# Performance work log

Hardware: AMD Instinct MI355X
Metric: run time of the kernel (lower is better)

Reference implementation:

```python
import jax, jax.numpy as jnp
import numpy as np


def setup_inputs() -> dict:
    key = jax.random.key(0)
    ks = jax.random.split(key, 8)
    B, C, H, W = 4, 128, 128, 128
    C8 = C // 8
    x = jax.random.normal(ks[0], (B, C, H, W), jnp.float32)
    # 1x1 conv weights as [out, in] matrices + biases
    Wq = jax.random.normal(ks[1], (C8, C), jnp.float32) * 0.05
    bq = jax.random.normal(ks[2], (C8,), jnp.float32) * 0.01
    Wk = jax.random.normal(ks[3], (C8, C), jnp.float32) * 0.05
    bk = jax.random.normal(ks[4], (C8,), jnp.float32) * 0.01
    Wv = jax.random.normal(ks[5], (C, C), jnp.float32) * 0.05
    bv = jax.random.normal(ks[6], (C,), jnp.float32) * 0.01
    # nn.Parameter(torch.zeros(1)) in the original; use nonzero so output/grads are nontrivial
    gamma = jax.random.normal(ks[7], (), jnp.float32) * 0.1
    return {"x": x, "Wq": Wq, "bq": bq, "Wk": Wk, "bk": bk,
            "Wv": Wv, "bv": bv, "gamma": gamma}


def reference(x, Wq, bq, Wk, bk, Wv, bv, gamma):
    # x: [b, c, h, w]
    b, c, h, w = x.shape
    # 1x1 convs == channel contractions
    q = jnp.einsum('bchw,oc->bohw', x, Wq) + bq[None, :, None, None]  # [b,c8,h,w]
    k = jnp.einsum('bchw,oc->bohw', x, Wk) + bk[None, :, None, None]  # [b,c8,h,w]
    v = jnp.einsum('bchw,oc->bohw', x, Wv) + bv[None, :, None, None]  # [b,c, h,w]

    # column (height) attention logits: e_h[b, h1, w, h2], diagonal masked to -inf
    e_h = jnp.einsum('bcxw,bcyw->bxwy', q, k)
    diag = jnp.eye(h, dtype=bool)  # [h1, h2]
    e_h = jnp.where(diag[:, None, :], -jnp.inf, e_h)
    # row (width) attention logits: e_w[b, h, w1, w2]
    e_w = jnp.einsum('bchx,bchy->bhxy', q, k)

    # joint softmax over concatenated (h2 + w2) axis
    attn = jax.nn.softmax(jnp.concatenate([e_h, e_w], axis=3), axis=3)  # [b,h,w,h+w]
    attn_h = attn[..., :h]   # [b, h1, w, h2]
    attn_w = attn[..., h:]   # [b, h, w1, w2]

    # aggregate values along columns and rows
    out_h = jnp.einsum('bcyw,bxwy->bcxw', v, attn_h)  # [b,c,h,w]
    out_w = jnp.einsum('bchy,bhxy->bchx', v, attn_w)  # [b,c,h,w]

    out = gamma * (out_h + out_w) + x
    # return_attn: stack([b h2 h1 w, b w2 h w1], dim=1)
    return_attn = jnp.stack([jnp.transpose(attn_h, (0, 3, 1, 2)),
                             jnp.transpose(attn_w, (0, 3, 1, 2))], axis=1)
    return out, return_attn
```

## Files before the change

kernel.cpp:

```cpp
#include <hip/hip_runtime.h>
#include <math.h>

#define HW_ 16384
#define SLOT_ 2097152ULL
#define BSTR_ 4194304ULL

typedef __attribute__((ext_vector_type(8))) short short8v;
typedef __attribute__((ext_vector_type(4))) float f32x4;

__device__ __forceinline__ unsigned short f2bf(float f) {
  unsigned int u = __float_as_uint(f);
  u = (u + 0x7FFFu + ((u >> 16) & 1u)) >> 16;
  return (unsigned short)u;
}
__device__ __forceinline__ float bf2f(unsigned short h) {
  return __uint_as_float(((unsigned int)h) << 16);
}

__global__ void __launch_bounds__(256, 2)
qkv_proj(const float* __restrict__ x,
         const float* __restrict__ Wq, const float* __restrict__ bq,
         const float* __restrict__ Wk, const float* __restrict__ bk,
         const float* __restrict__ Wv, const float* __restrict__ bv,
         float* __restrict__ qT, float* __restrict__ kT,
         unsigned short* __restrict__ vA0,
         unsigned short* __restrict__ Ew, float* __restrict__ rsw) {
  __shared__ unsigned short LDSU[39168];
  unsigned short (*WqkL)[136] = (unsigned short(*)[136])LDSU;
  unsigned short (*WvL)[136]  = (unsigned short(*)[136])(LDSU + 4352);
  unsigned short (*XT)[136]   = (unsigned short(*)[136])(LDSU + 21760);
  int t = threadIdx.x;
  int blk = blockIdx.x;
  int b = blk >> 7, h = blk & 127;
  {
    int och = t >> 3, kb = (t & 7) * 16;
    const float* src = (och < 16 ? Wq + och * 128 : Wk + (och - 16) * 128) + kb;
    union { unsigned short us[8]; uint4 v; } p0, p1;
#pragma unroll
    for (int j = 0; j < 8; ++j) p0.us[j] = f2bf(src[j]);
#pragma unroll
    for (int j = 0; j < 8; ++j) p1.us[j] = f2bf(src[8 + j]);
    *(uint4*)&WqkL[och][kb]     = p0.v;
    *(uint4*)&WqkL[och][kb + 8] = p1.v;
  }
  {
    int c = t >> 1, kb = (t & 1) * 64;
    const float* src = Wv + c * 128 + kb;
#pragma unroll
    for (int g = 0; g < 8; ++g) {
      union { unsigned short us[8]; uint4 v; } p;
#pragma unroll
      for (int j = 0; j < 8; ++j) p.us[j] = f2bf(src[g * 8 + j]);
      *(uint4*)&WvL[c][kb + g * 8] = p.v;
    }
  }
  {
    int k = t >> 1, pxb = (t & 1) * 64;
    const float* src = x + (size_t)b * 128 * HW_ + (size_t)k * HW_ + h * 128 + pxb;
#pragma unroll
    for (int j = 0; j < 64; ++j)
      XT[pxb + j][k] = f2bf(src[j]);
  }
  int wv = t >> 6, l = t & 63;
  int lm = l & 15, lk = (l >> 4) * 4, lr4 = (l >> 4) * 4;
  int wc = (wv >> 1) * 64, wx = (wv & 1) * 64;
  int ocht = (wv >> 1) * 16;
  float bvr[4][4];
#pragma unroll
  for (int mi = 0; mi < 4; ++mi)
#pragma unroll
    for (int r = 0; r < 4; ++r) bvr[mi][r] = bv[wc + mi * 16 + lr4 + r];
  float bqk[4];
#pragma unroll
  for (int r = 0; r < 4; ++r) {
    int och = ocht + lr4 + r;
    bqk[r] = (och < 16) ? bq[och] : bk[och - 16];
  }
  f32x4 acc[4][4];
#pragma unroll
  for (int mi = 0; mi < 4; ++mi)
#pragma unroll
    for (int ni = 0; ni < 4; ++ni) acc[mi][ni] = (f32x4){0.f, 0.f, 0.f, 0.f};
  f32x4 acc2[4];
#pragma unroll
  for (int ni = 0; ni < 4; ++ni) acc2[ni] = (f32x4){0.f, 0.f, 0.f, 0.f};
  __syncthreads();
  for (int y0 = 0; y0 < 128; y0 += 32) {
    short8v bf[4];
#pragma unroll
    for (int ni = 0; ni < 4; ++ni) {
      const unsigned short* bp = &XT[wx + ni * 16 + lm][y0 + lk];
      union { uint2 p[2]; short8v v; } u;
      u.p[0] = *(const uint2*)bp;
      u.p[1] = *(const uint2*)(bp + 16);
      bf[ni] = u.v;
    }
#pragma unroll
    for (int mi = 0; mi < 4; ++mi) {
      const unsigned short* ap = &WvL[wc + mi * 16 + lm][y0 + lk];
      union { uint2 p[2]; short8v v; } u;
      u.p[0] = *(const uint2*)ap;
      u.p[1] = *(const uint2*)(ap + 16);
      short8v af = u.v;
#pragma unroll
      for (int ni = 0; ni < 4; ++ni)
        acc[mi][ni] = __builtin_amdgcn_mfma_f32_16x16x32_bf16(af, bf[ni], acc[mi][ni], 0, 0, 0);
    }
    {
      const unsigned short* ap = &WqkL[ocht + lm][y0 + lk];
      union { uint2 p[2]; short8v v; } u;
      u.p[0] = *(const uint2*)ap;
      u.p[1] = *(const uint2*)(ap + 16);
      short8v aq = u.v;
#pragma unroll
      for (int ni = 0; ni < 4; ++ni)
        acc2[ni] = __builtin_amdgcn_mfma_f32_16x16x32_bf16(aq, bf[ni], acc2[ni], 0, 0, 0);
    }
  }
#pragma unroll
  for (int ni = 0; ni < 4; ++ni) {
    int px = wx + ni * 16 + lm;
#pragma unroll
    for (int mi = 0; mi < 4; ++mi)
#pragma unroll
      for (int r = 0; r < 4; ++r) {
        int c = wc + mi * 16 + lr4 + r;
        vA0[(size_t)(b * 128 + h) * 16384 + (size_t)c * 128 + px] =
            f2bf(acc[mi][ni][r] + bvr[mi][r]);
      }
  }
  __syncthreads();
  float (*QKs)[36] = (float(*)[36])(LDSU + 21760);
#pragma unroll
  for (int ni = 0; ni < 4; ++ni) {
    int px = (wv & 1) * 64 + ni * 16 + lm;
#pragma unroll
    for (int r = 0; r < 4; ++r)
      QKs[px][ocht + lr4 + r] = acc2[ni][r] + bqk[r];
  }
  __syncthreads();
  {
    int px_ = t >> 1, sel = t & 1;
    const float* qr = &QKs[px_][sel * 16];
    float4 r0 = *(const float4*)(qr);
    float4 r1 = *(const float4*)(qr + 4);
    float4 r2 = *(const float4*)(qr + 8);
    float4 r3 = *(const float4*)(qr + 12);
    float* dstT = (sel ? kT : qT) + ((size_t)(b * HW_ + px_ * 128 + h)) * 16;
    *(float4*)(dstT)      = r0;
    *(float4*)(dstT + 4)  = r1;
    *(float4*)(dstT + 8)  = r2;
    *(float4*)(dstT + 12) = r3;
  }
  float (*Qs)[132] = (float(*)[132])(LDSU + 4352);
  float (*Ks)[132] = (float(*)[132])(LDSU + 8576);
  {
    int cc = t & 15, pb = (t >> 4) * 8;
#pragma unroll
    for (int u = 0; u < 8; ++u) {
      Qs[cc][pb + u] = QKs[pb + u][cc];
      Ks[cc][pb + u] = QKs[pb + u][16 + cc];
    }
  }
  __syncthreads();
  {
    int tr = (t >> 4) * 8;
    int ty = (t & 15) * 8;
    float sc_[8][8] = {{0.f}};
#pragma unroll
    for (int c = 0; c < 16; ++c) {
      float qa[8], ka[8];
      *(float4*)(qa)     = *(const float4*)&Qs[c][tr];
      *(float4*)(qa + 4) = *(const float4*)&Qs[c][tr + 4];
      *(float4*)(ka)     = *(const float4*)&Ks[c][ty];
      *(float4*)(ka + 4) = *(const float4*)&Ks[c][ty + 4];
#pragma unroll
      for (int u = 0; u < 8; ++u)
#pragma unroll
        for (int v = 0; v < 8; ++v)
          sc_[u][v] = fmaf(qa[u], ka[v], sc_[u][v]);
    }
    float rp[8];
#pragma unroll
    for (int u = 0; u < 8; ++u) {
      rp[u] = 0.f;
#pragma unroll
      for (int v = 0; v < 8; ++v) {
        float e = __expf(sc_[u][v]);
        sc_[u][v] = e;
        rp[u] += e;
      }
    }
    unsigned short* out = Ew + (size_t)blk * 16384;
#pragma unroll
    for (int u = 0; u < 8; ++u) {
      union { unsigned short us[8]; uint4 v; } pk;
#pragma unroll
      for (int v = 0; v < 8; ++v) pk.us[v] = f2bf(sc_[u][v]);
      *(uint4*)&out[(tr + u) * 128 + ty] = pk.v;
    }
#pragma unroll
    for (int u = 0; u < 8; ++u) {
      rp[u] += __shfl_xor(rp[u], 1);
      rp[u] += __shfl_xor(rp[u], 2);
      rp[u] += __shfl_xor(rp[u], 4);
      rp[u] += __shfl_xor(rp[u], 8);
    }
    if ((t & 15) == 0) {
#pragma unroll
      for (int u = 0; u < 8; ++u) rsw[(size_t)blk * 128 + tr + u] = rp[u];
    }
  }
}

__global__ void score_h(const float* __restrict__ Q, const float* __restrict__ K,
                        unsigned short* __restrict__ E, float* __restrict__ rsum,
                        size_t ebs, size_t eoff) {
  __shared__ float Qs[16][132];
  __shared__ float Ks[16][132];
  int slab = blockIdx.x;
  int b = slab >> 7, s = slab & 127;
  const float* qb = Q + (size_t)slab * 2048;
  const float* kb = K + (size_t)slab * 2048;
  int t = threadIdx.x;
  int cc = t & 15;
  int pb = (t >> 4) * 8;
#pragma unroll
  for (int u = 0; u < 8; ++u) {
    Qs[cc][pb + u] = qb[(size_t)(pb + u) * 16 + cc];
    Ks[cc][pb + u] = kb[(size_t)(pb + u) * 16 + cc];
  }
  __syncthreads();
  int tr = (t >> 4) * 8;
  int ty = (t & 15) * 8;
  float acc[8][8] = {{0.f}};
#pragma unroll
  for (int c = 0; c < 16; ++c) {
    float qa[8], ka[8];
    *(float4*)(qa)     = *(const float4*)&Qs[c][tr];
    *(float4*)(qa + 4) = *(const float4*)&Qs[c][tr + 4];
    *(float4*)(ka)     = *(const float4*)&Ks[c][ty];
    *(float4*)(ka + 4) = *(const float4*)&Ks[c][ty + 4];
#pragma unroll
    for (int u = 0; u < 8; ++u)
#pragma unroll
      for (int v = 0; v < 8; ++v)
        acc[u][v] = fmaf(qa[u], ka[v], acc[u][v]);
  }
  float rp[8];
#pragma unroll
  for (int u = 0; u < 8; ++u) {
    rp[u] = 0.f;
#pragma unroll
    for (int v = 0; v < 8; ++v) {
      float e = __expf(acc[u][v]);
      if ((tr + u) == (ty + v)) e = 0.f;
      acc[u][v] = e;
      rp[u] += e;
    }
  }
  unsigned short* out = E + (size_t)b * ebs + eoff + (size_t)s * 16384;
#pragma unroll
  for (int u = 0; u < 8; ++u) {
    union { unsigned short us[8]; uint4 v; } pk;
#pragma unroll
    for (int v = 0; v < 8; ++v) pk.us[v] = f2bf(acc[u][v]);
    *(uint4*)&out[(tr + u) * 128 + ty] = pk.v;
  }
#pragma unroll
  for (int u = 0; u < 8; ++u) {
    rp[u] += __shfl_xor(rp[u], 1);
    rp[u] += __shfl_xor(rp[u], 2);
    rp[u] += __shfl_xor(rp[u], 4);
    rp[u] += __shfl_xor(rp[u], 8);
  }
  if ((t & 15) == 0) {
#pragma unroll
    for (int u = 0; u < 8; ++u) rsum[(size_t)slab * 128 + tr + u] = rp[u];
  }
}

__global__ void trans_v(const unsigned short* __restrict__ vA0, unsigned short* __restrict__ vA1,
                        const float* __restrict__ rsw, const float* __restrict__ rsh,
                        float* __restrict__ dij, float* __restrict__ dji) {
  __shared__ unsigned short tile[64][65];
  int blk = blockIdx.x;
  int q = blk & 3, c = (blk >> 2) & 127, b = blk >> 9;
  int h0 = (q >> 1) * 64, w0 = (q & 1) * 64;
  int t = threadIdx.x, lane = t & 63, r0 = (t >> 6) * 16;
  for (int r = r0; r < r0 + 16; ++r)
    tile[r][lane] = vA0[(size_t)(b * 128 + h0 + r) * 16384 + c * 128 + w0 + lane];
  __syncthreads();
  for (int r = r0; r < r0 + 16; ++r)
    vA1[(size_t)(b * 128 + w0 + r) * 16384 + c * 128 + h0 + lane] = tile[lane][r];
  if (blk < 256) {
    int p = blk * 256 + t;
    int bb = p >> 14, rem = p & 16383, i = rem >> 7, j = rem & 127;
    float d = rsw[p] + rsh[(size_t)bb * HW_ + j * 128 + i];
    float r = 1.0f / d;
    dij[p] = r;
    dji[(size_t)bb * HW_ + j * 128 + i] = r;
  }
}

__global__ void pv2(const unsigned short* __restrict__ vA0,
                    const unsigned short* __restrict__ vA1,
                    const unsigned short* __restrict__ Ew,
                    const unsigned short* __restrict__ EhB,
                    const float* __restrict__ dij, const float* __restrict__ dji,
                    unsigned short* __restrict__ ow, unsigned short* __restrict__ ohb) {
  __shared__ unsigned short Al[128][44];
  __shared__ unsigned short Bl[128][44];
  int blk = blockIdx.x;
  int m = blk >> 9;
  int slab = blk & 511;
  int s = slab & 127, b = slab >> 7;
  int t = threadIdx.x;
  int wv = t >> 6, l = t & 63;
  int wc = (wv >> 1) * 64, wx = (wv & 1) * 64;
  const unsigned short* vs = (m ? vA1 : vA0) + (size_t)slab * 16384;
  const unsigned short* es = m ? (EhB + (size_t)b * 8388608 + 4194304 + (size_t)s * 16384)
                               : (Ew + (size_t)slab * 16384);
  const float* invd = m ? dji : dij;
  f32x4 acc[4][4];
#pragma unroll
  for (int mi = 0; mi < 4; ++mi)
#pragma unroll
    for (int ni = 0; ni < 4; ++ni) acc[mi][ni] = (f32x4){0.f, 0.f, 0.f, 0.f};
  int lrow = t >> 2, lq = t & 3;
  int lm = l & 15, lk = (l >> 4) * 4;
  for (int y0 = 0; y0 < 128; y0 += 32) {
#pragma unroll
    for (int r = 0; r < 2; ++r) {
      int rr = lrow + r * 64;
      uint4 av = *(const uint4*)(vs + (size_t)rr * 128 + y0 + lq * 8);
      uint4 bv = *(const uint4*)(es + (size_t)rr * 128 + y0 + lq * 8);
      *(uint2*)&Al[rr][lq * 8]     = make_uint2(av.x, av.y);
      *(uint2*)&Al[rr][lq * 8 + 4] = make_uint2(av.z, av.w);
      *(uint2*)&Bl[rr][lq * 8]     = make_uint2(bv.x, bv.y);
      *(uint2*)&Bl[rr][lq * 8 + 4] = make_uint2(bv.z, bv.w);
    }
    __syncthreads();
    short8v af[4], bf[4];
#pragma unroll
    for (int mi = 0; mi < 4; ++mi) {
      const unsigned short* ap = &Al[wc + mi * 16 + lm][lk];
      union { uint2 p[2]; short8v v; } u;
      u.p[0] = *(const uint2*)ap;
      u.p[1] = *(const uint2*)(ap + 16);
      af[mi] = u.v;
    }
#pragma unroll
    for (int ni = 0; ni < 4; ++ni) {
      const unsigned short* bp = &Bl[wx + ni * 16 + lm][lk];
      union { uint2 p[2]; short8v v; } u;
      u.p[0] = *(const uint2*)bp;
      u.p[1] = *(const uint2*)(bp + 16);
      bf[ni] = u.v;
    }
#pragma unroll
    for (int mi = 0; mi < 4; ++mi)
#pragma unroll
      for (int ni = 0; ni < 4; ++ni)
        acc[mi][ni] = __builtin_amdgcn_mfma_f32_16x16x32_bf16(af[mi], bf[ni], acc[mi][ni], 0, 0, 0);
    __syncthreads();
  }
  int lr4 = (l >> 4) * 4;
  unsigned short* dst = m ? ohb : ow;
#pragma unroll
  for (int ni = 0; ni < 4; ++ni) {
    int xx = wx + ni * 16 + lm;
    float idv = invd[(size_t)(b * 128 + s) * 128 + xx];
#pragma unroll
    for (int mi = 0; mi < 4; ++mi) {
#pragma unroll
      for (int r = 0; r < 4; ++r) {
        int c = wc + mi * 16 + lr4 + r;
        size_t idx = m ? ((size_t)b * 8388608 + (size_t)s * 16384 + (size_t)c * 128 + xx)
                       : ((((size_t)(b * 128 + c)) * 128 + s) * 128 + xx);
        dst[idx] = f2bf(acc[mi][ni][r] * idv);
      }
    }
  }
}

__global__ void merge2(const unsigned short* __restrict__ ow,
                       const unsigned short* __restrict__ ohp,
                       const float* __restrict__ xin, const float* __restrict__ gamma,
                       float* __restrict__ outp) {
  __shared__ float tile[64][65];
  int blk = blockIdx.x;
  int q = blk & 3, c = (blk >> 2) & 127, b = blk >> 9;
  int h0 = (q >> 1) * 64, w0 = (q & 1) * 64;
  int t = threadIdx.x, lane = t & 63, r0 = (t >> 6) * 16;
  for (int r = r0; r < r0 + 16; ++r)
    tile[r][lane] =
        bf2f(ohp[(size_t)b * 8388608ULL + (size_t)(w0 + r) * 16384 + c * 128 + h0 + lane]);
  __syncthreads();
  float g = gamma[0];
  for (int r = r0; r < r0 + 16; ++r) {
    size_t a = (((size_t)(b * 128 + c)) * 128 + h0 + r) * 128 + w0 + lane;
    outp[a] = g * (bf2f(ow[a]) + tile[lane][r]) + xin[a];
  }
}

template <int HM>
__global__ void ret_write(const unsigned short* __restrict__ src, const float* __restrict__ invd,
                          float* __restrict__ retb, size_t sbs, size_t soff) {
  __shared__ float tile[128][129];
  __shared__ float idv[128];
  int slab = blockIdx.x;
  int b = slab >> 7, i = slab & 127;
  int t = threadIdx.x;
  const unsigned short* sp = src + (size_t)b * sbs + soff;
#pragma unroll
  for (int r = 0; r < 8; ++r) {
    int idx = r * 2048 + t * 8;
    int j = idx >> 7, y = idx & 127;
    uint4 raw;
    if (HM == 0)
      raw = *(const uint4*)(sp + (size_t)i * 16384 + j * 128 + y);
    else
      raw = *(const uint4*)(sp + (size_t)j * 16384 + i * 128 + y);
    unsigned int wd[4] = {raw.x, raw.y, raw.z, raw.w};
#pragma unroll
    for (int e = 0; e < 4; ++e) {
      tile[j][y + 2 * e]     = __uint_as_float((wd[e] & 0xFFFFu) << 16);
      tile[j][y + 2 * e + 1] = __uint_as_float(wd[e] & 0xFFFF0000u);
    }
  }
  if (t < 128) idv[t] = invd[(size_t)slab * 128 + t];
  __syncthreads();
  float* dp = retb + (size_t)b * BSTR_ + (HM == 0 ? SLOT_ : 0);
#pragma unroll
  for (int r = 0; r < 16; ++r) {
    int idx = r * 1024 + t * 4;
    int y = idx >> 7, j = idx & 127;
    float4 o;
    o.x = tile[j][y]     * idv[j];
    o.y = tile[j + 1][y] * idv[j + 1];
    o.z = tile[j + 2][y] * idv[j + 2];
    o.w = tile[j + 3][y] * idv[j + 3];
    *(float4*)&dp[(size_t)y * 16384 + i * 128 + j] = o;
  }
}

extern "C" void kernel_launch(void* const* d_in, const int* in_sizes, int n_in,
                              void* d_out, int out_size, void* d_ws, size_t ws_size,
                              hipStream_t stream) {
  const float* x     = (const float*)d_in[0];
  const float* Wq    = (const float*)d_in[1];
  const float* bq    = (const float*)d_in[2];
  const float* Wk    = (const float*)d_in[3];
  const float* bk    = (const float*)d_in[4];
  const float* Wv    = (const float*)d_in[5];
  const float* bv    = (const float*)d_in[6];
  const float* gamma = (const float*)d_in[7];

  float* outp = (float*)d_out;
  float* retb = outp + (size_t)8388608;
  unsigned short* ohb = (unsigned short*)retb;
  unsigned short* ehb = (unsigned short*)retb;

  float* ws      = (float*)d_ws;
  float* qT      = ws + (size_t)2097152;
  float* kT      = ws + (size_t)3145728;
  unsigned short* ow  = (unsigned short*)ws;
  unsigned short* vA0 = (unsigned short*)(ws + (size_t)4194304);
  unsigned short* vA1 = (unsigned short*)(ws + (size_t)8388608);
  unsigned short* E_w = (unsigned short*)(ws + (size_t)12582912);
  float* rsum_w  = ws + (size_t)16777216;
  float* rsum_h  = ws + (size_t)16842752;
  float* invd_ij = ws + (size_t)16908288;
  float* invd_ji = ws + (size_t)16973824;

  qkv_proj<<<512, 256, 0, stream>>>(x, Wq, bq, Wk, bk, Wv, bv,
                                    qT, kT, vA0, E_w, rsum_w);
  score_h<<<512, 256, 0, stream>>>(qT, kT, ehb, rsum_h,
                                   (size_t)8388608, (size_t)4194304);
  trans_v<<<2048, 256, 0, stream>>>(vA0, vA1, rsum_w, rsum_h, invd_ij, invd_ji);
  pv2<<<1024, 256, 0, stream>>>(vA0, vA1, E_w, ehb, invd_ij, invd_ji, ow, ohb);
  merge2<<<2048, 256, 0, stream>>>(ow, ohb, x, gamma, outp);
  ret_write<1><<<512, 256, 0, stream>>>(ehb, invd_ij, retb, (size_t)8388608, (size_t)4194304);
  ret_write<0><<<512, 256, 0, stream>>>(E_w, invd_ij, retb, (size_t)2097152, (size_t)0);
}
```

Before: 111.7 us.

## Merge V transpose into score kernel, compute inverse denominators inline, stage stores

Merges the score_h and V-transpose kernels into one launch, dispatching on block index. This removes one kernel launch and lets the two independent jobs run concurrently. The inverse-denominator precompute is dropped, and pv2 and ret_write now compute 1/(rsum_w+rsum_h) per slab directly from the row sums. The scattered per-element bf16 stores in qkv_proj and pv2 are replaced with LDS staging followed by coalesced 16-byte writes. This adds extra syncthreads and LDS traffic, plus some strided rsum reads.

Result: no change. 112.9 us (+1.0%).

```diff
diff --git a/kernel.cpp b/kernel.cpp
--- a/kernel.cpp
+++ b/kernel.cpp
@@ -117,17 +117,25 @@
         acc2[ni] = __builtin_amdgcn_mfma_f32_16x16x32_bf16(aq, bf[ni], acc2[ni], 0, 0, 0);
     }
   }
+  __syncthreads();
+  unsigned short (*VL)[136] = (unsigned short(*)[136])(LDSU + 21760);
 #pragma unroll
   for (int ni = 0; ni < 4; ++ni) {
     int px = wx + ni * 16 + lm;
 #pragma unroll
     for (int mi = 0; mi < 4; ++mi)
 #pragma unroll
-      for (int r = 0; r < 4; ++r) {
-        int c = wc + mi * 16 + lr4 + r;
-        vA0[(size_t)(b * 128 + h) * 16384 + (size_t)c * 128 + px] =
-            f2bf(acc[mi][ni][r] + bvr[mi][r]);
-      }
+      for (int r = 0; r < 4; ++r)
+        VL[wc + mi * 16 + lr4 + r][px] = f2bf(acc[mi][ni][r] + bvr[mi][r]);
+  }
+  __syncthreads();
+  {
+    int c = t >> 1, pxb = (t & 1) * 64;
+    unsigned short* dst = vA0 + (size_t)(b * 128 + h) * 16384 + (size_t)c * 128 + pxb;
+    const unsigned short* srcl = &VL[c][pxb];
+#pragma unroll
+    for (int g = 0; g < 8; ++g)
+      *(uint4*)(dst + g * 8) = *(const uint4*)(srcl + g * 8);
   }
   __syncthreads();
   float (*QKs)[36] = (float(*)[36])(LDSU + 21760);
@@ -213,16 +221,29 @@
   }
 }
 
-__global__ void score_h(const float* __restrict__ Q, const float* __restrict__ K,
-                        unsigned short* __restrict__ E, float* __restrict__ rsum,
-                        size_t ebs, size_t eoff) {
+__global__ void aux_k(const unsigned short* __restrict__ vA0, unsigned short* __restrict__ vA1,
+                      const float* __restrict__ Q, const float* __restrict__ K,
+                      unsigned short* __restrict__ EhB, float* __restrict__ rsum) {
+  __shared__ unsigned short tile[64][65];
   __shared__ float Qs[16][132];
   __shared__ float Ks[16][132];
-  int slab = blockIdx.x;
+  int blk = blockIdx.x;
+  int t = threadIdx.x;
+  if (blk < 2048) {
+    int q = blk & 3, c = (blk >> 2) & 127, b = blk >> 9;
+    int h0 = (q >> 1) * 64, w0 = (q & 1) * 64;
+    int lane = t & 63, r0 = (t >> 6) * 16;
+    for (int r = r0; r < r0 + 16; ++r)
+      tile[r][lane] = vA0[(size_t)(b * 128 + h0 + r) * 16384 + c * 128 + w0 + lane];
+    __syncthreads();
+    for (int r = r0; r < r0 + 16; ++r)
+      vA1[(size_t)(b * 128 + w0 + r) * 16384 + c * 128 + h0 + lane] = tile[lane][r];
+    return;
+  }
+  int slab = blk - 2048;
   int b = slab >> 7, s = slab & 127;
   const float* qb = Q + (size_t)slab * 2048;
   const float* kb = K + (size_t)slab * 2048;
-  int t = threadIdx.x;
   int cc = t & 15;
   int pb = (t >> 4) * 8;
 #pragma unroll
@@ -259,7 +280,7 @@
       rp[u] += e;
     }
   }
-  unsigned short* out = E + (size_t)b * ebs + eoff + (size_t)s * 16384;
+  unsigned short* out = EhB + (size_t)b * 8388608 + 4194304 + (size_t)s * 16384;
 #pragma unroll
   for (int u = 0; u < 8; ++u) {
     union { unsigned short us[8]; uint4 v; } pk;
@@ -280,48 +301,31 @@
   }
 }
 
-__global__ void trans_v(const unsigned short* __restrict__ vA0, unsigned short* __restrict__ vA1,
-                        const float* __restrict__ rsw, const float* __restrict__ rsh,
-                        float* __restrict__ dij, float* __restrict__ dji) {
-  __shared__ unsigned short tile[64][65];
-  int blk = blockIdx.x;
-  int q = blk & 3, c = (blk >> 2) & 127, b = blk >> 9;
-  int h0 = (q >> 1) * 64, w0 = (q & 1) * 64;
-  int t = threadIdx.x, lane = t & 63, r0 = (t >> 6) * 16;
-  for (int r = r0; r < r0 + 16; ++r)
-    tile[r][lane] = vA0[(size_t)(b * 128 + h0 + r) * 16384 + c * 128 + w0 + lane];
-  __syncthreads();
-  for (int r = r0; r < r0 + 16; ++r)
-    vA1[(size_t)(b * 128 + w0 + r) * 16384 + c * 128 + h0 + lane] = tile[lane][r];
-  if (blk < 256) {
-    int p = blk * 256 + t;
-    int bb = p >> 14, rem = p & 16383, i = rem >> 7, j = rem & 127;
-    float d = rsw[p] + rsh[(size_t)bb * HW_ + j * 128 + i];
-    float r = 1.0f / d;
-    dij[p] = r;
-    dji[(size_t)bb * HW_ + j * 128 + i] = r;
-  }
-}
-
 __global__ void pv2(const unsigned short* __restrict__ vA0,
                     const unsigned short* __restrict__ vA1,
                     const unsigned short* __restrict__ Ew,
                     const unsigned short* __restrict__ EhB,
-                    const float* __restrict__ dij, const float* __restrict__ dji,
+                    const float* __restrict__ rsw, const float* __restrict__ rsh,
                     unsigned short* __restrict__ ow, unsigned short* __restrict__ ohb) {
-  __shared__ unsigned short Al[128][44];
-  __shared__ unsigned short Bl[128][44];
+  __shared__ unsigned short UB[17408];
+  __shared__ float idvs[128];
+  unsigned short (*Al)[44] = (unsigned short(*)[44])UB;
+  unsigned short (*Bl)[44] = (unsigned short(*)[44])(UB + 5632);
   int blk = blockIdx.x;
   int m = blk >> 9;
   int slab = blk & 511;
   int s = slab & 127, b = slab >> 7;
   int t = threadIdx.x;
+  if (t < 128) {
+    const float* rc = m ? rsh : rsw;
+    const float* rg = m ? rsw : rsh;
+    idvs[t] = 1.0f / (rc[(size_t)(b * 128 + s) * 128 + t] + rg[(size_t)b * HW_ + t * 128 + s]);
+  }
   int wv = t >> 6, l = t & 63;
   int wc = (wv >> 1) * 64, wx = (wv & 1) * 64;
   const unsigned short* vs = (m ? vA1 : vA0) + (size_t)slab * 16384;
   const unsigned short* es = m ? (EhB + (size_t)b * 8388608 + 4194304 + (size_t)s * 16384)
                                : (Ew + (size_t)slab * 16384);
-  const float* invd = m ? dji : dij;
   f32x4 acc[4][4];
 #pragma unroll
   for (int mi = 0; mi < 4; ++mi)
@@ -365,22 +369,28 @@
         acc[mi][ni] = __builtin_amdgcn_mfma_f32_16x16x32_bf16(af[mi], bf[ni], acc[mi][ni], 0, 0, 0);
     __syncthreads();
   }
+  unsigned short (*OutS)[136] = (unsigned short(*)[136])UB;
   int lr4 = (l >> 4) * 4;
-  unsigned short* dst = m ? ohb : ow;
 #pragma unroll
   for (int ni = 0; ni < 4; ++ni) {
     int xx = wx + ni * 16 + lm;
-    float idv = invd[(size_t)(b * 128 + s) * 128 + xx];
-#pragma unroll
-    for (int mi = 0; mi < 4; ++mi) {
-#pragma unroll
-      for (int r = 0; r < 4; ++r) {
-        int c = wc + mi * 16 + lr4 + r;
-        size_t idx = m ? ((size_t)b * 8388608 + (size_t)s * 16384 + (size_t)c * 128 + xx)
-                       : ((((size_t)(b * 128 + c)) * 128 + s) * 128 + xx);
-        dst[idx] = f2bf(acc[mi][ni][r] * idv);
-      }
-    }
+    float idv = idvs[xx];
+#pragma unroll
+    for (int mi = 0; mi < 4; ++mi)
+#pragma unroll
+      for (int r = 0; r < 4; ++r)
+        OutS[wc + mi * 16 + lr4 + r][xx] = f2bf(acc[mi][ni][r] * idv);
+  }
+  __syncthreads();
+  {
+    int c = t >> 1, xb = (t & 1) * 64;
+    unsigned short* dst = m
+        ? (ohb + (size_t)b * 8388608 + (size_t)s * 16384 + (size_t)c * 128 + xb)
+        : (ow + (((size_t)(b * 128 + c)) * 128 + s) * 128 + xb);
+    const unsigned short* srcl = &OutS[c][xb];
+#pragma unroll
+    for (int g = 0; g < 8; ++g)
+      *(uint4*)(dst + g * 8) = *(const uint4*)(srcl + g * 8);
   }
 }
 
@@ -405,7 +415,8 @@
 }
 
 template <int HM>
-__global__ void ret_write(const unsigned short* __restrict__ src, const float* __restrict__ invd,
+__global__ void ret_write(const unsigned short* __restrict__ src,
+                          const float* __restrict__ rsw, const float* __restrict__ rsh,
                           float* __restrict__ retb, size_t sbs, size_t soff) {
   __shared__ float tile[128][129];
   __shared__ float idv[128];
@@ -429,7 +440,8 @@
       tile[j][y + 2 * e + 1] = __uint_as_float(wd[e] & 0xFFFF0000u);
     }
   }
-  if (t < 128) idv[t] = invd[(size_t)slab * 128 + t];
+  if (t < 128)
+    idv[t] = 1.0f / (rsw[(size_t)(b * 128 + i) * 128 + t] + rsh[(size_t)b * HW_ + t * 128 + i]);
   __syncthreads();
   float* dp = retb + (size_t)b * BSTR_ + (HM == 0 ? SLOT_ : 0);
 #pragma unroll
@@ -471,16 +483,14 @@
   unsigned short* E_w = (unsigned short*)(ws + (size_t)12582912);
   float* rsum_w  = ws + (size_t)16777216;
   float* rsum_h  = ws + (size_t)16842752;
-  float* invd_ij = ws + (size_t)16908288;
-  float* invd_ji = ws + (size_t)16973824;
 
   qkv_proj<<<512, 256, 0, stream>>>(x, Wq, bq, Wk, bk, Wv, bv,
                                     qT, kT, vA0, E_w, rsum_w);
-  score_h<<<512, 256, 0, stream>>>(qT, kT, ehb, rsum_h,
-                                   (size_t)8388608, (size_t)4194304);
-  trans_v<<<2048, 256, 0, stream>>>(vA0, vA1, rsum_w, rsum_h, invd_ij, invd_ji);
-  pv2<<<1024, 256, 0, stream>>>(vA0, vA1, E_w, ehb, invd_ij, invd_ji, ow, ohb);
+  aux_k<<<2560, 256, 0, stream>>>(vA0, vA1, qT, kT, (unsigned short*)retb, rsum_h);
+  pv2<<<1024, 256, 0, stream>>>(vA0, vA1, E_w, ehb, rsum_w, rsum_h, ow, ohb);
   merge2<<<2048, 256, 0, stream>>>(ow, ohb, x, gamma, outp);
-  ret_write<1><<<512, 256, 0, stream>>>(ehb, invd_ij, retb, (size_t)8388608, (size_t)4194304);
-  ret_write<0><<<512, 256, 0, stream>>>(E_w, invd_ij, retb, (size_t)2097152, (size_t)0);
-}
+  ret_write<1><<<512, 256, 0, stream>>>(ehb, rsum_w, rsum_h, retb,
+                                        (size_t)8388608, (size_t)4194304);
+  ret_write<0><<<512, 256, 0, stream>>>(E_w, rsum_w, rsum_h, retb,
+                                        (size_t)2097152, (size_t)0);
+}
```
